# Kernel tuning notes

Measured on AMD Instinct MI355X. Metric: run time of the kernel, lower is better.

Reference implementation:

```python
import jax, jax.numpy as jnp
import numpy as np

N = 200_000   # total nodes across batched AIGs
E = 400_000   # edges (fan-in ~2 per gate)
D = 64        # input_dim == dim_hidden (required by in-place scatter in _gru_forward)
B = 16        # number of graphs in batch
LF = 12       # num forward topological levels
LB = 12       # num backward topological levels
NUM_ROUNDS = 1


def setup_inputs() -> dict:
    key = jax.random.key(0)
    ks = jax.random.split(key, 9)
    node_type = jax.random.randint(ks[0], (N,), 0, 3, dtype=jnp.int32)
    num_inverted_predecessors = jax.random.randint(ks[1], (N,), 0, 3, dtype=jnp.int32)
    edge_index = jax.random.randint(ks[2], (2, E), 0, N, dtype=jnp.int32)
    forward_level = jax.random.randint(ks[3], (N,), 0, LF, dtype=jnp.int32)
    backward_level = jax.random.randint(ks[4], (N,), 0, LB, dtype=jnp.int32)
    batch = jnp.sort(jax.random.randint(ks[5], (N,), 0, B, dtype=jnp.int32))
    s = 1.0 / np.sqrt(D)
    W_enc = jax.random.normal(ks[6], (2, D), dtype=jnp.float32) * 0.5
    b_enc = jnp.zeros((D,), dtype=jnp.float32)
    W_f = jax.random.normal(ks[7], (D, D), dtype=jnp.float32) * s
    b_f = jnp.zeros((D,), dtype=jnp.float32)
    W_b = jax.random.normal(ks[8], (D, D), dtype=jnp.float32) * s
    b_b = jnp.zeros((D,), dtype=jnp.float32)
    return dict(node_type=node_type,
                num_inverted_predecessors=num_inverted_predecessors,
                edge_index=edge_index,
                forward_level=forward_level,
                backward_level=backward_level,
                batch=batch,
                W_enc=W_enc, b_enc=b_enc,
                W_f=W_f, b_f=b_f,
                W_b=W_b, b_b=b_b)


def reference(node_type, num_inverted_predecessors, edge_index,
              forward_level, backward_level, batch,
              W_enc, b_enc, W_f, b_f, W_b, b_b):
    # h_init = node_encoder(cat(node_type, num_inverted_predecessors))
    x = jnp.stack([node_type, num_inverted_predecessors], axis=1).astype(W_enc.dtype)  # [N,2]
    h = x @ W_enc + b_enc  # [N,D] node_state
    src, dst = edge_index[0], edge_index[1]

    for _ in range(NUM_ROUNDS):
        # forward topological sweep: level l nodes receive sum of mlp(h_src)
        # over incoming edges whose destination is at level l (subgraph dim=1).
        for l in range(1, LF):
            m = h @ W_f + b_f                                    # AggConv mlp on current state
            e_w = (forward_level[dst] == l).astype(h.dtype)      # edges into level-l nodes
            msg = jax.ops.segment_sum(m[src] * e_w[:, None], dst, num_segments=N)
            h = jnp.where((forward_level == l)[:, None], msg, h)  # scatter l_msg into node_state
        # backward sweep (reverse flow): level-l sources receive sum of
        # mlp_b(h_dst) over outgoing edges (subgraph dim=0, target_to_source).
        for l in range(1, LB):
            m = h @ W_b + b_b
            e_w = (backward_level[src] == l).astype(h.dtype)
            msg = jax.ops.segment_sum(m[dst] * e_w[:, None], src, num_segments=N)
            h = jnp.where((backward_level == l)[:, None], msg, h)

    # readout over output nodes (node_type == 1): [global_max_pool, global_add_pool]
    out_mask = (node_type == 1)
    neg_inf = jnp.finfo(h.dtype).min
    max_pool = jax.ops.segment_max(jnp.where(out_mask[:, None], h, neg_inf), batch, num_segments=B)
    sum_pool = jax.ops.segment_sum(h * out_mask[:, None].astype(h.dtype), batch, num_segments=B)
    return jnp.concatenate([max_pool, sum_pool], axis=1)  # [B, 2*D]
```

## Files before the change

### kernel.cpp

```cpp
#include <hip/hip_runtime.h>
#include <float.h>

#define NLVL 12
#define NB   16
#define NBLK 256
#define EBLK 2048
#define SWBLK 1024


struct Params {
    const int *nt, *ninv, *src, *dst, *fl, *bl, *batch;
    const float *We, *be, *Wf, *bf, *Wb, *bb;
    float *hN, *hB, *tabg, *out;
    int *rowptr, *cursor, *col, *nb_f, *nb_b, *onodes, *bsums, *meta, *plarr, *bar;
    int *cntf, *cntb, *cnto, *blkf, *blkb, *blko;
    int N, E, M, outN;
};

__device__ __forceinline__ float rlanef(float x, int l) {
    return __int_as_float(__builtin_amdgcn_readlane(__float_as_int(x), l));
}

__device__ __forceinline__ void gbar3(int* bar, int nblk, int t) {
    __syncthreads();
    if (threadIdx.x == 0) {
        const int line = blockIdx.x & 15;
        const int per  = nblk >> 4;
        int a = __hip_atomic_fetch_add(&bar[line * 32], 1,
                                       __ATOMIC_RELAXED, __HIP_MEMORY_SCOPE_AGENT);
        if (a == per * t - 1) {
            int m = __hip_atomic_fetch_add(&bar[16 * 32], 1,
                                           __ATOMIC_RELAXED, __HIP_MEMORY_SCOPE_AGENT);
            if (m == 16 * t - 1) {
                __hip_atomic_store(&bar[17 * 32], t,
                                   __ATOMIC_RELAXED, __HIP_MEMORY_SCOPE_AGENT);
            } else {
                while (__hip_atomic_load(&bar[17 * 32], __ATOMIC_RELAXED,
                                         __HIP_MEMORY_SCOPE_AGENT) < t)
                    __builtin_amdgcn_s_sleep(1);
            }
            for (int b = line; b < nblk; b += 16)
                __hip_atomic_store(&bar[(18 + b) * 32], t,
                                   __ATOMIC_RELAXED, __HIP_MEMORY_SCOPE_AGENT);
        } else {
            while (__hip_atomic_load(&bar[(18 + blockIdx.x) * 32], __ATOMIC_RELAXED,
                                     __HIP_MEMORY_SCOPE_AGENT) < t)
                __builtin_amdgcn_s_sleep(4);
        }
    }
    asm volatile("" ::: "memory");
    __syncthreads();
}

__global__ void k_edge_deg(Params p) {
    int g = blockIdx.x * 256 + threadIdx.x, gs = gridDim.x * 256;
    for (int e = g; e < p.E; e += gs) {
        atomicAdd(&p.rowptr[p.dst[e]], 1);
        atomicAdd(&p.rowptr[p.N + p.src[e]], 1);
    }
}

__global__ void k_deg_hist(Params p) {
    __shared__ int hf[NLVL], hb[NLVL], ho[NB];
    int tid = threadIdx.x, bid = blockIdx.x;
    if (tid < NLVL) { hf[tid] = 0; hb[tid] = 0; }
    if (tid < NB) ho[tid] = 0;
    __syncthreads();
    int chunk = (p.N + gridDim.x - 1) / gridDim.x;
    int lo = bid * chunk, hi = lo + chunk; if (hi > p.N) hi = p.N;
    for (int i = lo + tid; i < hi; i += 256) {
        int f = p.fl[i], b = p.bl[i];
        int t = p.nt[i], iv = p.ninv[i];
        p.plarr[i] = f | (b << 4) | ((t * 3 + iv) << 8);
        atomicAdd(&hf[f], 1);
        atomicAdd(&hb[b], 1);
        if (t == 1) atomicAdd(&ho[p.batch[i]], 1);
    }
    __syncthreads();
    if (tid < NLVL) { p.cntf[tid * NBLK + bid] = hf[tid]; p.cntb[tid * NBLK + bid] = hb[tid]; }
    if (tid < NB) p.cnto[tid * NBLK + bid] = ho[tid];
}

__global__ void k_scan1(int* __restrict__ data, int M, int* __restrict__ bsums) {
    __shared__ int s[512];
    int t = threadIdx.x;
    int g = blockIdx.x * 512 + t;
    int v = (g < M) ? data[g] : 0;
    s[t] = v;
    __syncthreads();
    for (int off = 1; off < 512; off <<= 1) {
        int add = (t >= off) ? s[t - off] : 0;
        __syncthreads();
        s[t] += add;
        __syncthreads();
    }
    if (g < M) data[g] = s[t] - v;
    if (t == 511) bsums[blockIdx.x] = s[511];
}

__global__ void k_scan_top(int* __restrict__ bsums, int nblk, Params p,
                           float* __restrict__ out, int outN) {
    __shared__ int s[1024];
    __shared__ int tot[48];
    int t = threadIdx.x;
    int* meta = p.meta;
    for (int i = t; i < outN; i += 1024)
        out[i] = ((i & 127) < 64) ? -FLT_MAX : 0.0f;
    if (t < 576) {
        int row = t >> 6, j = t & 63;
        float nf = (float)(row / 3), iv = (float)(row % 3);
        p.tabg[t] = fmaf(nf, p.We[j], fmaf(iv, p.We[64 + j], p.be[j]));
    }
    int seg = t >> 8, b = t & 255;
    for (int r = 0; r < 3; r++) {
        int l = 4 * r + seg;
        int v = p.cntf[l * NBLK + b];
        s[t] = v; __syncthreads();
        for (int off = 1; off < NBLK; off <<= 1) {
            int add = (b >= off) ? s[t - off] : 0; __syncthreads();
            s[t] += add; __syncthreads();
        }
        p.blkf[l * NBLK + b] = s[t] - v;
        if (b == NBLK - 1) tot[l] = s[t];
        __syncthreads();
    }
    for (int r = 0; r < 3; r++) {
        int l = 4 * r + seg;
        int v = p.cntb[l * NBLK + b];
        s[t] = v; __syncthreads();
        for (int off = 1; off < NBLK; off <<= 1) {
            int add = (b >= off) ? s[t - off] : 0; __syncthreads();
            s[t] += add; __syncthreads();
        }
        p.blkb[l * NBLK + b] = s[t] - v;
        if (b == NBLK - 1) tot[16 + l] = s[t];
        __syncthreads();
    }
    for (int r = 0; r < 4; r++) {
        int l = 4 * r + seg;
        int v = p.cnto[l * NBLK + b];
        s[t] = v; __syncthreads();
        for (int off = 1; off < NBLK; off <<= 1) {
            int add = (b >= off) ? s[t - off] : 0; __syncthreads();
            s[t] += add; __syncthreads();
        }
        p.blko[l * NBLK + b] = s[t] - v;
        if (b == NBLK - 1) tot[32 + l] = s[t];
        __syncthreads();
    }
    if (t == 0) { int a = 0; for (int l = 0; l < NLVL; l++) { meta[96 + l] = a; a += tot[l]; } meta[96 + NLVL] = a; }
    if (t == 1) { int a = 0; for (int l = 0; l < NLVL; l++) { meta[128 + l] = a; a += tot[16 + l]; } meta[128 + NLVL] = a; }
    if (t == 2) { int a = 0; for (int l = 0; l < NB; l++) { meta[160 + l] = a; a += tot[32 + l]; } meta[160 + NB] = a; }
    __syncthreads();
    for (int i = t; i < NLVL * NBLK; i += 1024) p.blkf[i] += meta[96 + (i >> 8)];
    for (int i = t; i < NLVL * NBLK; i += 1024) p.blkb[i] += meta[128 + (i >> 8)];
    for (int i = t; i < NB * NBLK; i += 1024) p.blko[i] += meta[160 + (i >> 8)];
    int v = (t < nblk) ? bsums[t] : 0;
    s[t] = v;
    __syncthreads();
    for (int off = 1; off < 1024; off <<= 1) {
        int add = (t >= off) ? s[t - off] : 0;
        __syncthreads();
        s[t] += add;
        __syncthreads();
    }
    if (t < nblk) bsums[t] = s[t] - v;
}

__global__ void k_scan_add(int* __restrict__ rowptr, int* __restrict__ cursor, int M, int total,
                           const int* __restrict__ bsums) {
    int g = blockIdx.x * blockDim.x + threadIdx.x;
    if (g >= M) return;
    int r = rowptr[g] + bsums[g >> 9];
    rowptr[g] = r;
    cursor[g] = r;
    if (g == 0) rowptr[M] = total;
}

__global__ void k_edge_fill(Params p) {
    int g = blockIdx.x * 256 + threadIdx.x, gs = gridDim.x * 256;
    int N = p.N;
    for (int e = g; e < p.E; e += gs) {
        int s = p.src[e], d = p.dst[e];
        p.col[atomicAdd(&p.cursor[d], 1)] = s | (p.plarr[s] << 18);
        p.col[atomicAdd(&p.cursor[N + s], 1)] = d | (p.plarr[d] << 18);
    }
}

__global__ void k_fill(Params p) {
    __shared__ int cur[48];
    int tid = threadIdx.x, bid = blockIdx.x;
    int N = p.N;
    if (tid < NLVL) { cur[tid] = p.blkf[tid * NBLK + bid]; cur[16 + tid] = p.blkb[tid * NBLK + bid]; }
    if (tid < NB) cur[32 + tid] = p.blko[tid * NBLK + bid];
    __syncthreads();
    int chunk = (N + gridDim.x - 1) / gridDim.x;
    int lo = bid * chunk, hi = lo + chunk; if (hi > N) hi = N;
    for (int i = lo + tid; i < hi; i += 256) {
        int pl = p.plarr[i];
        int lf = pl & 15, lb = (pl >> 4) & 15, tx = (pl >> 8) & 15;
        int pk = i | (pl << 18);
        p.nb_f[atomicAdd(&cur[lf], 1)] = pk;
        p.nb_b[atomicAdd(&cur[16 + lb], 1)] = pk;
        if (tx >= 3 && tx < 6)
            p.onodes[atomicAdd(&cur[32 + p.batch[i]], 1)] = pk;
    }
}

template <int DIR>
__device__ __forceinline__ void sweep_level(const Params& p, int lvl,
                                            const float (&w)[64], float bv,
                                            int lane, int wid, int nw, int q, int fb) {
    const int* nb = DIR ? p.nb_b : p.nb_f;
    const int* rp = p.rowptr + (DIR ? p.N : 0);
    int start = p.meta[(DIR ? 128 : 96) + lvl];
    int cnt   = p.meta[(DIR ? 128 : 96) + lvl + 1] - start;
    float* db = DIR ? p.hB : p.hN;

    int c0 = (int)((long long)cnt * wid / nw);
    int c1 = (int)((long long)cnt * (wid + 1) / nw);
    for (int i = c0; i < c1; i += 4) {
        int my = i + q;
        int v = 0, rpv = 0, rpe = 0;
        if (my < c1) {
            int e = nb[start + my];
            v = e & 0x3FFFF;
            rpv = rp[v]; rpe = rp[v + 1];
        }
        float4 acc = make_float4(0.f, 0.f, 0.f, 0.f);
        for (int cb = rpv; cb < rpe; cb++) {
            int cu = p.col[cb];
            int u = cu & 0x3FFFF;
            int flu = (cu >> 18) & 15, blu = (cu >> 22) & 15;
            const float* sp;
            if (DIR == 0)
                sp = (flu > 0 && flu < lvl) ? (p.hN + (size_t)u * 64)
                                            : (p.tabg + ((cu >> 26) & 15) * 64);
            else
                sp = (blu > 0 && blu < lvl) ? (p.hB + (size_t)u * 64)
                   : (flu > 0)              ? (p.hN + (size_t)u * 64)
                                            : (p.tabg + ((cu >> 26) & 15) * 64);
            const float4 x = *(const float4*)(sp + fb);
            acc.x += x.x; acc.y += x.y; acc.z += x.z; acc.w += x.w;
        }
        #pragma unroll
        for (int qq = 0; qq < 4; qq++) {
            if (i + qq >= c1) break;
            int vs   = __builtin_amdgcn_readlane(v, 16 * qq);
            int degs = __builtin_amdgcn_readlane(rpe, 16 * qq)
                     - __builtin_amdgcn_readlane(rpv, 16 * qq);
            float o = bv * (float)degs;
            #pragma unroll
            for (int m = 0; m < 16; m++) {
                float ax = rlanef(acc.x, 16 * qq + m);
                float ay = rlanef(acc.y, 16 * qq + m);
                float az = rlanef(acc.z, 16 * qq + m);
                float aw = rlanef(acc.w, 16 * qq + m);
                o = fmaf(ax, w[4 * m + 0], o);
                o = fmaf(ay, w[4 * m + 1], o);
                o = fmaf(az, w[4 * m + 2], o);
                o = fmaf(aw, w[4 * m + 3], o);
            }
            __hip_atomic_store(&db[(size_t)vs * 64 + lane], o,
                               __ATOMIC_RELAXED, __HIP_MEMORY_SCOPE_AGENT);
        }
    }
}

__global__ __launch_bounds__(256) __attribute__((amdgpu_waves_per_eu(4, 4)))
void k_sweep_all(Params p) {
    const int tid = threadIdx.x, lane = tid & 63;
    const int wid = (blockIdx.x * 256 + tid) >> 6;
    const int nw  = (gridDim.x * 256) >> 6;
    const int q = lane >> 4, fb = (lane & 15) * 4;
    int* bar = p.bar;
    const int nblk = gridDim.x;
    int t = 0;

    {
        float w[64];
        #pragma unroll
        for (int k = 0; k < 64; k++) w[k] = p.Wf[k * 64 + lane];
        float bv = p.bf[lane];
        for (int lvl = 1; lvl < NLVL; lvl++) {
            sweep_level<0>(p, lvl, w, bv, lane, wid, nw, q, fb);
            gbar3(bar, nblk, ++t);
        }
    }
    {
        float w[64];
        #pragma unroll
        for (int k = 0; k < 64; k++) w[k] = p.Wb[k * 64 + lane];
        float bv = p.bb[lane];
        for (int lvl = 1; lvl < NLVL; lvl++) {
            sweep_level<1>(p, lvl, w, bv, lane, wid, nw, q, fb);
            if (lvl < NLVL - 1) gbar3(bar, nblk, ++t);
        }
    }
}

__global__ __launch_bounds__(256) __attribute__((amdgpu_waves_per_eu(4, 4)))
void k_sweep(Params p, int lvl, int dir) {
    const int tid = threadIdx.x, lane = tid & 63;
    const float* W = dir ? p.Wb : p.Wf;
    float w[64];
    #pragma unroll
    for (int k = 0; k < 64; k++) w[k] = W[k * 64 + lane];
    float bv = (dir ? p.bb : p.bf)[lane];
    const int wid = (blockIdx.x * 256 + tid) >> 6;
    const int nw  = (gridDim.x * 256) >> 6;
    const int q = lane >> 4, fb = (lane & 15) * 4;
    if (dir == 0) sweep_level<0>(p, lvl, w, bv, lane, wid, nw, q, fb);
    else          sweep_level<1>(p, lvl, w, bv, lane, wid, nw, q, fb);
}

__device__ inline void atomicMaxF(float* addr, float val) {
    int* ai = (int*)addr;
    int old = *ai;
    while (__int_as_float(old) < val) {
        int assumed = old;
        old = atomicCAS(ai, assumed, __float_as_int(val));
        if (old == assumed) break;
    }
}

__global__ void k_readout(Params p) {
    int lane = threadIdx.x & 63;
    int b = blockIdx.x >> 5;
    int sl = blockIdx.x & 31;
    int a0 = p.meta[160 + b], a1 = p.meta[161 + b];
    int cnt = a1 - a0;
    if (cnt == 0) return;
    int lo = a0 + (int)((long long)cnt * sl / 32);
    int hi = a0 + (int)((long long)cnt * (sl + 1) / 32);
    int wcnt = hi - lo;
    int wave = threadIdx.x >> 6;
    int wl = lo + (wcnt * wave) / 4;
    int wh = lo + (wcnt * (wave + 1)) / 4;
    if (wh <= wl) return;
    float mx = -FLT_MAX, sm = 0.f;
    for (int k = wl; k < wh; k += 64) {
        int take = wh - k; if (take > 64) take = 64;
        int el = (lane < take) ? p.onodes[k + lane] : 0;
        for (int j = 0; j < take; j++) {
            int e = __shfl(el, j, 64);
            int v = e & 0x3FFFF;
            int flv = (e >> 18) & 15, blv = (e >> 22) & 15;
            const float* sp = (blv > 0) ? (p.hB + (size_t)v * 64)
                            : (flv > 0) ? (p.hN + (size_t)v * 64)
                                        : (p.tabg + ((e >> 26) & 15) * 64);
            float x = sp[lane];
            mx = fmaxf(mx, x);
            sm += x;
        }
    }
    atomicMaxF(&p.out[b * 128 + lane], mx);
    atomicAdd(&p.out[b * 128 + 64 + lane], sm);
}

extern "C" void kernel_launch(void* const* d_in, const int* in_sizes, int n_in,
                              void* d_out, int out_size, void* d_ws, size_t ws_size,
                              hipStream_t stream) {
    int N = in_sizes[0];
    int E = in_sizes[2] / 2;
    int M = 2 * N;

    Params p;
    p.nt    = (const int*)d_in[0];
    p.ninv  = (const int*)d_in[1];
    p.src   = (const int*)d_in[2];
    p.dst   = (const int*)d_in[2] + E;
    p.fl    = (const int*)d_in[3];
    p.bl    = (const int*)d_in[4];
    p.batch = (const int*)d_in[5];
    p.We    = (const float*)d_in[6];
    p.be    = (const float*)d_in[7];
    p.Wf    = (const float*)d_in[8];
    p.bf    = (const float*)d_in[9];
    p.Wb    = (const float*)d_in[10];
    p.bb    = (const float*)d_in[11];
    p.out   = (float*)d_out;
    p.N = N; p.E = E; p.M = M; p.outN = out_size;

    char* ws = (char*)d_ws;
    size_t off = 0;
    auto alloc = [&](size_t bytes) -> char* {
        char* q = ws + off;
        off = (off + bytes + 255) & ~(size_t)255;
        return q;
    };
    p.rowptr = (int*)  alloc((size_t)(M + 1) * sizeof(int));
    p.meta   = (int*)  alloc(256 * sizeof(int));
    p.bar    = (int*)  alloc((size_t)(18 + SWBLK) * 32 * sizeof(int));
    size_t zbytes = (size_t)((char*)(p.bar + (18 + SWBLK) * 32) - (char*)p.rowptr);
    p.hN     = (float*)alloc((size_t)N * 64 * sizeof(float));
    p.hB     = (float*)alloc((size_t)N * 64 * sizeof(float));
    p.tabg   = (float*)alloc(9 * 64 * sizeof(float));
    p.cursor = (int*)  alloc((size_t)M * sizeof(int));
    p.col    = (int*)  alloc((size_t)2 * E * sizeof(int));
    p.nb_f   = (int*)  alloc((size_t)N * sizeof(int));
    p.nb_b   = (int*)  alloc((size_t)N * sizeof(int));
    p.onodes = (int*)  alloc((size_t)N * sizeof(int));
    p.plarr  = (int*)  alloc((size_t)N * sizeof(int));
    p.bsums  = (int*)  alloc(1024 * sizeof(int));
    p.cntf   = (int*)  alloc(NLVL * NBLK * sizeof(int));
    p.cntb   = (int*)  alloc(NLVL * NBLK * sizeof(int));
    p.cnto   = (int*)  alloc(NB * NBLK * sizeof(int));
    p.blkf   = (int*)  alloc(NLVL * NBLK * sizeof(int));
    p.blkb   = (int*)  alloc(NLVL * NBLK * sizeof(int));
    p.blko   = (int*)  alloc(NB * NBLK * sizeof(int));

    int nscan = (M + 511) / 512;

    hipMemsetAsync(p.rowptr, 0, zbytes, stream);
    k_edge_deg<<<EBLK, 256, 0, stream>>>(p);
    k_deg_hist<<<NBLK, 256, 0, stream>>>(p);
    k_scan1<<<nscan, 512, 0, stream>>>(p.rowptr, M, p.bsums);
    k_scan_top<<<1, 1024, 0, stream>>>(p.bsums, nscan, p, p.out, out_size);
    k_scan_add<<<(M + 255) / 256, 256, 0, stream>>>(p.rowptr, p.cursor, M, 2 * E, p.bsums);
    k_edge_fill<<<EBLK, 256, 0, stream>>>(p);
    k_fill<<<NBLK, 256, 0, stream>>>(p);

    static int g_swgrid = -2;
    if (g_swgrid == -2) {
        int mb = 0;
        if (hipOccupancyMaxActiveBlocksPerMultiprocessor(&mb, k_sweep_all, 256, 0)
                == hipSuccess && mb > 0) {
            int dev = 0;
            hipGetDevice(&dev);
            hipDeviceProp_t props;
            if (hipGetDeviceProperties(&props, dev) == hipSuccess) {
                long cap = (long)mb * props.multiProcessorCount;
                long g = cap < SWBLK ? cap : SWBLK;
                g &= ~15L;
                g_swgrid = (g >= 16) ? (int)g : -1;
            } else g_swgrid = -1;
        } else g_swgrid = -1;
    }

    bool launched = false;
    if (g_swgrid >= 16) {
        k_sweep_all<<<g_swgrid, 256, 0, stream>>>(p);
        launched = true;
    } else {
        void* kargs[] = { (void*)&p };
        launched = hipLaunchCooperativeKernel((const void*)k_sweep_all, dim3(SWBLK),
                                              dim3(256), kargs, 0, stream) == hipSuccess;
    }
    if (!launched) {
        for (int l = 1; l < NLVL; l++)
            k_sweep<<<1024, 256, 0, stream>>>(p, l, 0);
        for (int l = 1; l < NLVL; l++)
            k_sweep<<<1024, 256, 0, stream>>>(p, l, 1);
    }

    k_readout<<<NB * 32, 256, 0, stream>>>(p);
}
```

Baseline: 560.0 us.

## Fuse edge fill, node fill, sweeps and readout into one persistent kernel

Folds the CSR edge fill, the per-level node list fill and the readout into the persistent sweep kernel, separated by the software grid barrier. This removes three kernel launches and their launch gaps. Writes before the barrier become agent-scope atomic stores so other blocks see them. It adds one more barrier, and the readout runs on only a subset of blocks after the final backward level, which now also ends in a barrier.

After: 542.9 us. 3.0% less time.

```diff
diff --git a/kernel.cpp b/kernel.cpp
--- a/kernel.cpp
+++ b/kernel.cpp
@@ -20,32 +20,36 @@
 __device__ __forceinline__ float rlanef(float x, int l) {
     return __int_as_float(__builtin_amdgcn_readlane(__float_as_int(x), l));
 }
+__device__ __forceinline__ void sti(int* a, int v) {
+    __hip_atomic_store(a, v, __ATOMIC_RELAXED, __HIP_MEMORY_SCOPE_AGENT);
+}
+__device__ __forceinline__ void stf(float* a, float v) {
+    __hip_atomic_store(a, v, __ATOMIC_RELAXED, __HIP_MEMORY_SCOPE_AGENT);
+}
+__device__ __forceinline__ int ald(int* a) {
+    return __hip_atomic_load(a, __ATOMIC_RELAXED, __HIP_MEMORY_SCOPE_AGENT);
+}
+__device__ __forceinline__ int afa(int* a, int v) {
+    return __hip_atomic_fetch_add(a, v, __ATOMIC_RELAXED, __HIP_MEMORY_SCOPE_AGENT);
+}
 
 __device__ __forceinline__ void gbar3(int* bar, int nblk, int t) {
     __syncthreads();
     if (threadIdx.x == 0) {
         const int line = blockIdx.x & 15;
         const int per  = nblk >> 4;
-        int a = __hip_atomic_fetch_add(&bar[line * 32], 1,
-                                       __ATOMIC_RELAXED, __HIP_MEMORY_SCOPE_AGENT);
+        int a = afa(&bar[line * 32], 1);
         if (a == per * t - 1) {
-            int m = __hip_atomic_fetch_add(&bar[16 * 32], 1,
-                                           __ATOMIC_RELAXED, __HIP_MEMORY_SCOPE_AGENT);
+            int m = afa(&bar[16 * 32], 1);
             if (m == 16 * t - 1) {
-                __hip_atomic_store(&bar[17 * 32], t,
-                                   __ATOMIC_RELAXED, __HIP_MEMORY_SCOPE_AGENT);
+                sti(&bar[17 * 32], t);
             } else {
-                while (__hip_atomic_load(&bar[17 * 32], __ATOMIC_RELAXED,
-                                         __HIP_MEMORY_SCOPE_AGENT) < t)
-                    __builtin_amdgcn_s_sleep(1);
+                while (ald(&bar[17 * 32]) < t) __builtin_amdgcn_s_sleep(1);
             }
             for (int b = line; b < nblk; b += 16)
-                __hip_atomic_store(&bar[(18 + b) * 32], t,
-                                   __ATOMIC_RELAXED, __HIP_MEMORY_SCOPE_AGENT);
+                sti(&bar[(18 + b) * 32], t);
         } else {
-            while (__hip_atomic_load(&bar[(18 + blockIdx.x) * 32], __ATOMIC_RELAXED,
-                                     __HIP_MEMORY_SCOPE_AGENT) < t)
-                __builtin_amdgcn_s_sleep(4);
+            while (ald(&bar[(18 + blockIdx.x) * 32]) < t) __builtin_amdgcn_s_sleep(4);
         }
     }
     asm volatile("" ::: "memory");
@@ -175,36 +179,6 @@
     rowptr[g] = r;
     cursor[g] = r;
     if (g == 0) rowptr[M] = total;
-}
-
-__global__ void k_edge_fill(Params p) {
-    int g = blockIdx.x * 256 + threadIdx.x, gs = gridDim.x * 256;
-    int N = p.N;
-    for (int e = g; e < p.E; e += gs) {
-        int s = p.src[e], d = p.dst[e];
-        p.col[atomicAdd(&p.cursor[d], 1)] = s | (p.plarr[s] << 18);
-        p.col[atomicAdd(&p.cursor[N + s], 1)] = d | (p.plarr[d] << 18);
-    }
-}
-
-__global__ void k_fill(Params p) {
-    __shared__ int cur[48];
-    int tid = threadIdx.x, bid = blockIdx.x;
-    int N = p.N;
-    if (tid < NLVL) { cur[tid] = p.blkf[tid * NBLK + bid]; cur[16 + tid] = p.blkb[tid * NBLK + bid]; }
-    if (tid < NB) cur[32 + tid] = p.blko[tid * NBLK + bid];
-    __syncthreads();
-    int chunk = (N + gridDim.x - 1) / gridDim.x;
-    int lo = bid * chunk, hi = lo + chunk; if (hi > N) hi = N;
-    for (int i = lo + tid; i < hi; i += 256) {
-        int pl = p.plarr[i];
-        int lf = pl & 15, lb = (pl >> 4) & 15, tx = (pl >> 8) & 15;
-        int pk = i | (pl << 18);
-        p.nb_f[atomicAdd(&cur[lf], 1)] = pk;
-        p.nb_b[atomicAdd(&cur[16 + lb], 1)] = pk;
-        if (tx >= 3 && tx < 6)
-            p.onodes[atomicAdd(&cur[32 + p.batch[i]], 1)] = pk;
-    }
 }
 
 template <int DIR>
@@ -261,57 +235,9 @@
                 o = fmaf(az, w[4 * m + 2], o);
                 o = fmaf(aw, w[4 * m + 3], o);
             }
-            __hip_atomic_store(&db[(size_t)vs * 64 + lane], o,
-                               __ATOMIC_RELAXED, __HIP_MEMORY_SCOPE_AGENT);
-        }
-    }
-}
-
-__global__ __launch_bounds__(256) __attribute__((amdgpu_waves_per_eu(4, 4)))
-void k_sweep_all(Params p) {
-    const int tid = threadIdx.x, lane = tid & 63;
-    const int wid = (blockIdx.x * 256 + tid) >> 6;
-    const int nw  = (gridDim.x * 256) >> 6;
-    const int q = lane >> 4, fb = (lane & 15) * 4;
-    int* bar = p.bar;
-    const int nblk = gridDim.x;
-    int t = 0;
-
-    {
-        float w[64];
-        #pragma unroll
-        for (int k = 0; k < 64; k++) w[k] = p.Wf[k * 64 + lane];
-        float bv = p.bf[lane];
-        for (int lvl = 1; lvl < NLVL; lvl++) {
-            sweep_level<0>(p, lvl, w, bv, lane, wid, nw, q, fb);
-            gbar3(bar, nblk, ++t);
-        }
-    }
-    {
-        float w[64];
-        #pragma unroll
-        for (int k = 0; k < 64; k++) w[k] = p.Wb[k * 64 + lane];
-        float bv = p.bb[lane];
-        for (int lvl = 1; lvl < NLVL; lvl++) {
-            sweep_level<1>(p, lvl, w, bv, lane, wid, nw, q, fb);
-            if (lvl < NLVL - 1) gbar3(bar, nblk, ++t);
-        }
-    }
-}
-
-__global__ __launch_bounds__(256) __attribute__((amdgpu_waves_per_eu(4, 4)))
-void k_sweep(Params p, int lvl, int dir) {
-    const int tid = threadIdx.x, lane = tid & 63;
-    const float* W = dir ? p.Wb : p.Wf;
-    float w[64];
-    #pragma unroll
-    for (int k = 0; k < 64; k++) w[k] = W[k * 64 + lane];
-    float bv = (dir ? p.bb : p.bf)[lane];
-    const int wid = (blockIdx.x * 256 + tid) >> 6;
-    const int nw  = (gridDim.x * 256) >> 6;
-    const int q = lane >> 4, fb = (lane & 15) * 4;
-    if (dir == 0) sweep_level<0>(p, lvl, w, bv, lane, wid, nw, q, fb);
-    else          sweep_level<1>(p, lvl, w, bv, lane, wid, nw, q, fb);
+            stf(&db[(size_t)vs * 64 + lane], o);
+        }
+    }
 }
 
 __device__ inline void atomicMaxF(float* addr, float val) {
@@ -324,17 +250,17 @@
     }
 }
 
-__global__ void k_readout(Params p) {
-    int lane = threadIdx.x & 63;
-    int b = blockIdx.x >> 5;
-    int sl = blockIdx.x & 31;
+__device__ __forceinline__ void readout_body(const Params& p, int bid, int tid) {
+    int lane = tid & 63;
+    int b = bid >> 5;
+    int sl = bid & 31;
     int a0 = p.meta[160 + b], a1 = p.meta[161 + b];
     int cnt = a1 - a0;
     if (cnt == 0) return;
     int lo = a0 + (int)((long long)cnt * sl / 32);
     int hi = a0 + (int)((long long)cnt * (sl + 1) / 32);
     int wcnt = hi - lo;
-    int wave = threadIdx.x >> 6;
+    int wave = tid >> 6;
     int wl = lo + (wcnt * wave) / 4;
     int wh = lo + (wcnt * (wave + 1)) / 4;
     if (wh <= wl) return;
@@ -356,6 +282,114 @@
     }
     atomicMaxF(&p.out[b * 128 + lane], mx);
     atomicAdd(&p.out[b * 128 + 64 + lane], sm);
+}
+
+__global__ __launch_bounds__(256) __attribute__((amdgpu_waves_per_eu(4, 4)))
+void k_tail(Params p) {
+    const int tid = threadIdx.x, bid = blockIdx.x;
+    const int lane = tid & 63;
+    int* bar = p.bar;
+    const int nblk = gridDim.x;
+    int ep = 0;
+    __shared__ int cur[48];
+
+    for (int e = bid * 256 + tid; e < p.E; e += nblk * 256) {
+        int sN = p.src[e], d = p.dst[e];
+        sti(&p.col[atomicAdd(&p.cursor[d], 1)],        sN | (p.plarr[sN] << 18));
+        sti(&p.col[atomicAdd(&p.cursor[p.N + sN], 1)],  d | (p.plarr[d]  << 18));
+    }
+    if (bid < NBLK) {
+        if (tid < NLVL) { cur[tid] = p.blkf[tid * NBLK + bid]; cur[16 + tid] = p.blkb[tid * NBLK + bid]; }
+        if (tid < NB) cur[32 + tid] = p.blko[tid * NBLK + bid];
+        __syncthreads();
+        int chunk = (p.N + NBLK - 1) / NBLK;
+        int lo = bid * chunk, hi = lo + chunk; if (hi > p.N) hi = p.N;
+        for (int i = lo + tid; i < hi; i += 256) {
+            int pl = p.plarr[i];
+            int lf = pl & 15, lb = (pl >> 4) & 15, tx = (pl >> 8) & 15;
+            int pk = i | (pl << 18);
+            sti(&p.nb_f[atomicAdd(&cur[lf], 1)], pk);
+            sti(&p.nb_b[atomicAdd(&cur[16 + lb], 1)], pk);
+            if (tx >= 3 && tx < 6)
+                sti(&p.onodes[atomicAdd(&cur[32 + p.batch[i]], 1)], pk);
+        }
+    }
+    gbar3(bar, nblk, ++ep);
+
+    const int wid = (bid * 256 + tid) >> 6;
+    const int nw  = (nblk * 256) >> 6;
+    const int q = lane >> 4, fb = (lane & 15) * 4;
+    {
+        float w[64];
+        #pragma unroll
+        for (int k = 0; k < 64; k++) w[k] = p.Wf[k * 64 + lane];
+        float bv = p.bf[lane];
+        for (int lvl = 1; lvl < NLVL; lvl++) {
+            sweep_level<0>(p, lvl, w, bv, lane, wid, nw, q, fb);
+            gbar3(bar, nblk, ++ep);
+        }
+    }
+    {
+        float w[64];
+        #pragma unroll
+        for (int k = 0; k < 64; k++) w[k] = p.Wb[k * 64 + lane];
+        float bv = p.bb[lane];
+        for (int lvl = 1; lvl < NLVL; lvl++) {
+            sweep_level<1>(p, lvl, w, bv, lane, wid, nw, q, fb);
+            gbar3(bar, nblk, ++ep);
+        }
+    }
+
+    if (bid < NB * 32) readout_body(p, bid, tid);
+}
+
+__global__ void k_edge_fill(Params p) {
+    int g = blockIdx.x * 256 + threadIdx.x, gs = gridDim.x * 256;
+    int N = p.N;
+    for (int e = g; e < p.E; e += gs) {
+        int s = p.src[e], d = p.dst[e];
+        p.col[atomicAdd(&p.cursor[d], 1)] = s | (p.plarr[s] << 18);
+        p.col[atomicAdd(&p.cursor[N + s], 1)] = d | (p.plarr[d] << 18);
+    }
+}
+
+__global__ void k_fill(Params p) {
+    __shared__ int cur[48];
+    int tid = threadIdx.x, bid = blockIdx.x;
+    int N = p.N;
+    if (tid < NLVL) { cur[tid] = p.blkf[tid * NBLK + bid]; cur[16 + tid] = p.blkb[tid * NBLK + bid]; }
+    if (tid < NB) cur[32 + tid] = p.blko[tid * NBLK + bid];
+    __syncthreads();
+    int chunk = (N + gridDim.x - 1) / gridDim.x;
+    int lo = bid * chunk, hi = lo + chunk; if (hi > N) hi = N;
+    for (int i = lo + tid; i < hi; i += 256) {
+        int pl = p.plarr[i];
+        int lf = pl & 15, lb = (pl >> 4) & 15, tx = (pl >> 8) & 15;
+        int pk = i | (pl << 18);
+        p.nb_f[atomicAdd(&cur[lf], 1)] = pk;
+        p.nb_b[atomicAdd(&cur[16 + lb], 1)] = pk;
+        if (tx >= 3 && tx < 6)
+            p.onodes[atomicAdd(&cur[32 + p.batch[i]], 1)] = pk;
+    }
+}
+
+__global__ __launch_bounds__(256) __attribute__((amdgpu_waves_per_eu(4, 4)))
+void k_sweep(Params p, int lvl, int dir) {
+    const int tid = threadIdx.x, lane = tid & 63;
+    const float* W = dir ? p.Wb : p.Wf;
+    float w[64];
+    #pragma unroll
+    for (int k = 0; k < 64; k++) w[k] = W[k * 64 + lane];
+    float bv = (dir ? p.bb : p.bf)[lane];
+    const int wid = (blockIdx.x * 256 + tid) >> 6;
+    const int nw  = (gridDim.x * 256) >> 6;
+    const int q = lane >> 4, fb = (lane & 15) * 4;
+    if (dir == 0) sweep_level<0>(p, lvl, w, bv, lane, wid, nw, q, fb);
+    else          sweep_level<1>(p, lvl, w, bv, lane, wid, nw, q, fb);
+}
+
+__global__ void k_readout(Params p) {
+    readout_body(p, blockIdx.x, threadIdx.x);
 }
 
 extern "C" void kernel_launch(void* const* d_in, const int* in_sizes, int n_in,
@@ -412,20 +446,12 @@
 
     int nscan = (M + 511) / 512;
 
-    hipMemsetAsync(p.rowptr, 0, zbytes, stream);
-    k_edge_deg<<<EBLK, 256, 0, stream>>>(p);
-    k_deg_hist<<<NBLK, 256, 0, stream>>>(p);
-    k_scan1<<<nscan, 512, 0, stream>>>(p.rowptr, M, p.bsums);
-    k_scan_top<<<1, 1024, 0, stream>>>(p.bsums, nscan, p, p.out, out_size);
-    k_scan_add<<<(M + 255) / 256, 256, 0, stream>>>(p.rowptr, p.cursor, M, 2 * E, p.bsums);
-    k_edge_fill<<<EBLK, 256, 0, stream>>>(p);
-    k_fill<<<NBLK, 256, 0, stream>>>(p);
-
-    static int g_swgrid = -2;
-    if (g_swgrid == -2) {
+    static int g_tail = -2;
+    if (g_tail == -2) {
         int mb = 0;
-        if (hipOccupancyMaxActiveBlocksPerMultiprocessor(&mb, k_sweep_all, 256, 0)
-                == hipSuccess && mb > 0) {
+        g_tail = -1;
+        if (hipOccupancyMaxActiveBlocksPerMultiprocessor(&mb, k_tail, 256, 0) == hipSuccess
+                && mb > 0) {
             int dev = 0;
             hipGetDevice(&dev);
             hipDeviceProp_t props;
@@ -433,26 +459,34 @@
                 long cap = (long)mb * props.multiProcessorCount;
                 long g = cap < SWBLK ? cap : SWBLK;
                 g &= ~15L;
-                g_swgrid = (g >= 16) ? (int)g : -1;
-            } else g_swgrid = -1;
-        } else g_swgrid = -1;
-    }
+                if (g >= NBLK) g_tail = (int)g;
+            }
+        }
+    }
+
+    hipMemsetAsync(p.rowptr, 0, zbytes, stream);
+    k_edge_deg<<<EBLK, 256, 0, stream>>>(p);
+    k_deg_hist<<<NBLK, 256, 0, stream>>>(p);
+    k_scan1<<<nscan, 512, 0, stream>>>(p.rowptr, M, p.bsums);
+    k_scan_top<<<1, 1024, 0, stream>>>(p.bsums, nscan, p, p.out, out_size);
+    k_scan_add<<<(M + 255) / 256, 256, 0, stream>>>(p.rowptr, p.cursor, M, 2 * E, p.bsums);
 
     bool launched = false;
-    if (g_swgrid >= 16) {
-        k_sweep_all<<<g_swgrid, 256, 0, stream>>>(p);
+    if (g_tail >= NBLK) {
+        k_tail<<<g_tail, 256, 0, stream>>>(p);
         launched = true;
     } else {
         void* kargs[] = { (void*)&p };
-        launched = hipLaunchCooperativeKernel((const void*)k_sweep_all, dim3(SWBLK),
+        launched = hipLaunchCooperativeKernel((const void*)k_tail, dim3(SWBLK),
                                               dim3(256), kargs, 0, stream) == hipSuccess;
     }
     if (!launched) {
+        k_edge_fill<<<EBLK, 256, 0, stream>>>(p);
+        k_fill<<<NBLK, 256, 0, stream>>>(p);
         for (int l = 1; l < NLVL; l++)
             k_sweep<<<1024, 256, 0, stream>>>(p, l, 0);
         for (int l = 1; l < NLVL; l++)
             k_sweep<<<1024, 256, 0, stream>>>(p, l, 1);
-    }
-
-    k_readout<<<NB * 32, 256, 0, stream>>>(p);
-}
+        k_readout<<<NB * 32, 256, 0, stream>>>(p);
+    }
+}
```
